# Kernel tuning notes

Measured on AMD Instinct MI355X. Metric: run time of the kernel, lower is better.

Reference implementation:

```python
import jax, jax.numpy as jnp
import numpy as np

B, N = 4096, 2048


def setup_inputs() -> dict:
    key = jax.random.key(0)
    k1, k2, k3 = jax.random.split(key, 3)
    target = jax.random.normal(k1, (B, N, 3), dtype=jnp.float32)
    source = jax.random.normal(k2, (B, N, 3), dtype=jnp.float32)
    weights = jax.random.uniform(k3, (B, N, 1), dtype=jnp.float32)
    return {"target": target, "source": source, "weights": weights}


def reference(target, source, weights):
    # Weighted means over the point axis (weights is not None branch of torch code;
    # the isnan mask is unused in that branch).
    wsum = jnp.sum(weights, axis=-2, keepdims=True) + 1e-8  # [B,1,1]
    mean_s = jnp.sum(source * weights, axis=-2, keepdims=True) / wsum  # [B,1,3]
    mean_t = jnp.sum(target * weights, axis=-2, keepdims=True) / wsum  # [B,1,3]
    xyz_tc = (target - mean_t) * weights  # weighted centered target [B,N,3]
    xyz_sc = source - mean_s              # centered source [B,N,3]
    # Cross-covariance: cov = xyz_tc^T @ xyz_sc -> [B,3,3]
    cov = jnp.einsum("bni,bnj->bij", xyz_tc, xyz_sc)
    u, s, vh = jnp.linalg.svd(cov, full_matrices=False)
    rot = u @ vh  # [B,3,3] (no reflection fix, matching original)
    t = jnp.swapaxes(mean_t, -1, -2) - rot @ jnp.swapaxes(mean_s, -1, -2)  # [B,3,1]
    T = jnp.zeros(target.shape[:-2] + (4, 4), dtype=target.dtype)
    T = T.at[..., :3, :3].set(rot)
    T = T.at[..., :3, 3:].set(t)
    T = T.at[..., 3, 3].set(jnp.asarray(1.0, target.dtype))
    return T
```

## Files before the change

### kernel.cpp

```cpp
#include <hip/hip_runtime.h>
#include <math.h>


constexpr int BN      = 2048;
constexpr int THREADS = 256;

__global__ __launch_bounds__(THREADS) void moments_kernel(
    const float* __restrict__ target,
    const float* __restrict__ source,
    const float* __restrict__ weights,
    float* __restrict__ ws)
{
    const int lane = threadIdx.x & 63;
    const int b    = (blockIdx.x * THREADS + threadIdx.x) >> 6;

    const float4* t4 = reinterpret_cast<const float4*>(target + (size_t)b * BN * 3);
    const float4* s4 = reinterpret_cast<const float4*>(source + (size_t)b * BN * 3);
    const float4* w4 = reinterpret_cast<const float4*>(weights + (size_t)b * BN);

    float acc[16];
#pragma unroll
    for (int i = 0; i < 16; ++i) acc[i] = 0.f;

#pragma unroll
    for (int it = 0; it < BN / (64 * 4); ++it) {
        const int g  = it * 64 + lane;
        float4 t0 = t4[g * 3 + 0], t1 = t4[g * 3 + 1], t2 = t4[g * 3 + 2];
        float4 s0 = s4[g * 3 + 0], s1 = s4[g * 3 + 1], s2 = s4[g * 3 + 2];
        float4 wv = w4[g];

        float tx[4] = {t0.x, t0.w, t1.z, t2.y};
        float ty[4] = {t0.y, t1.x, t1.w, t2.z};
        float tz[4] = {t0.z, t1.y, t2.x, t2.w};
        float sx[4] = {s0.x, s0.w, s1.z, s2.y};
        float sy[4] = {s0.y, s1.x, s1.w, s2.z};
        float sz[4] = {s0.z, s1.y, s2.x, s2.w};
        float ww[4] = {wv.x, wv.y, wv.z, wv.w};

#pragma unroll
        for (int j = 0; j < 4; ++j) {
            float w = ww[j];
            acc[0] += w;
            float wtx = w * tx[j], wty = w * ty[j], wtz = w * tz[j];
            acc[1] += wtx;  acc[2] += wty;  acc[3] += wtz;
            acc[4] += w * sx[j]; acc[5] += w * sy[j]; acc[6] += w * sz[j];
            acc[7]  += wtx * sx[j]; acc[8]  += wtx * sy[j]; acc[9]  += wtx * sz[j];
            acc[10] += wty * sx[j]; acc[11] += wty * sy[j]; acc[12] += wty * sz[j];
            acc[13] += wtz * sx[j]; acc[14] += wtz * sy[j]; acc[15] += wtz * sz[j];
        }
    }

#pragma unroll
    for (int i = 0; i < 16; ++i) {
#pragma unroll
        for (int off = 32; off > 0; off >>= 1)
            acc[i] += __shfl_xor(acc[i], off);
    }

    if (lane == 0) {
        float4* o = reinterpret_cast<float4*>(ws + (size_t)b * 16);
        o[0] = make_float4(acc[0],  acc[1],  acc[2],  acc[3]);
        o[1] = make_float4(acc[4],  acc[5],  acc[6],  acc[7]);
        o[2] = make_float4(acc[8],  acc[9],  acc[10], acc[11]);
        o[3] = make_float4(acc[12], acc[13], acc[14], acc[15]);
    }
}

__global__ __launch_bounds__(64) void polar_kernel(
    const float* __restrict__ ws,
    float* __restrict__ out,
    int B)
{
    const int b = blockIdx.x * 64 + threadIdx.x;
    if (b >= B) return;

    const float4* i4 = reinterpret_cast<const float4*>(ws + (size_t)b * 16);
    float4 p0 = i4[0], p1 = i4[1], p2 = i4[2], p3 = i4[3];
    double v[16] = {p0.x, p0.y, p0.z, p0.w,  p1.x, p1.y, p1.z, p1.w,
                    p2.x, p2.y, p2.z, p2.w,  p3.x, p3.y, p3.z, p3.w};

    const double W  = v[0];
    const double Wd = W + 1e-8;
    double St[3] = {v[1], v[2], v[3]};
    double Ss[3] = {v[4], v[5], v[6]};
    double mt[3], ms[3];
#pragma unroll
    for (int i = 0; i < 3; ++i) { mt[i] = St[i] / Wd; ms[i] = Ss[i] / Wd; }

    double A[3][3];
#pragma unroll
    for (int i = 0; i < 3; ++i)
#pragma unroll
        for (int j = 0; j < 3; ++j)
            A[i][j] = v[7 + i * 3 + j] - mt[i] * Ss[j] - ms[j] * St[i] + mt[i] * ms[j] * W;

    double X[3][3];
#pragma unroll
    for (int i = 0; i < 3; ++i)
#pragma unroll
        for (int j = 0; j < 3; ++j) X[i][j] = A[i][j];

#pragma unroll
    for (int iter = 0; iter < 12; ++iter) {
        double C[3][3];
        C[0][0] = X[1][1]*X[2][2] - X[1][2]*X[2][1];
        C[0][1] = X[1][2]*X[2][0] - X[1][0]*X[2][2];
        C[0][2] = X[1][0]*X[2][1] - X[1][1]*X[2][0];
        C[1][0] = X[0][2]*X[2][1] - X[0][1]*X[2][2];
        C[1][1] = X[0][0]*X[2][2] - X[0][2]*X[2][0];
        C[1][2] = X[0][1]*X[2][0] - X[0][0]*X[2][1];
        C[2][0] = X[0][1]*X[1][2] - X[0][2]*X[1][1];
        C[2][1] = X[0][2]*X[1][0] - X[0][0]*X[1][2];
        C[2][2] = X[0][0]*X[1][1] - X[0][1]*X[1][0];
        double det = X[0][0]*C[0][0] + X[0][1]*C[0][1] + X[0][2]*C[0][2];
        double ad  = fabs(det);
        if (!(ad > 1e-300)) { det = (det >= 0.0) ? 1e-300 : -1e-300; ad = 1e-300; }

        double mu = 1.0;
        if (iter < 9) {
            float adf = (float)ad;
            if (adf > 0.f && isfinite(adf))
                mu = (double)exp2f(-log2f(adf) * (1.0f / 3.0f));
        }
        double k1 = 0.5 * mu;
        double k2 = 0.5 / (mu * det);
#pragma unroll
        for (int i = 0; i < 3; ++i)
#pragma unroll
            for (int j = 0; j < 3; ++j)
                X[i][j] = k1 * X[i][j] + k2 * C[i][j];
    }

    double tvec[3];
#pragma unroll
    for (int i = 0; i < 3; ++i) {
        double s = mt[i];
#pragma unroll
        for (int k = 0; k < 3; ++k) s -= X[i][k] * ms[k];
        tvec[i] = s;
    }

    float4* o = reinterpret_cast<float4*>(out + (size_t)b * 16);
    o[0] = make_float4((float)X[0][0], (float)X[0][1], (float)X[0][2], (float)tvec[0]);
    o[1] = make_float4((float)X[1][0], (float)X[1][1], (float)X[1][2], (float)tvec[1]);
    o[2] = make_float4((float)X[2][0], (float)X[2][1], (float)X[2][2], (float)tvec[2]);
    o[3] = make_float4(0.f, 0.f, 0.f, 1.f);
}

extern "C" void kernel_launch(void* const* d_in, const int* in_sizes, int n_in,
                              void* d_out, int out_size, void* d_ws, size_t ws_size,
                              hipStream_t stream) {
    const float* target  = (const float*)d_in[0];
    const float* source  = (const float*)d_in[1];
    const float* weights = (const float*)d_in[2];
    float* out = (float*)d_out;
    float* ws  = (float*)d_ws;

    const int B = in_sizes[2] / BN;

    moments_kernel<<<B / (THREADS / 64), THREADS, 0, stream>>>(target, source, weights, ws);
    polar_kernel<<<(B + 63) / 64, 64, 0, stream>>>(ws, out, B);
}
```

Baseline: 43.57 us.

## Split each batch's point reduction across two wavefronts with a transpose-style shuffle reduce

```diff
diff --git a/kernel.cpp b/kernel.cpp
--- a/kernel.cpp
+++ b/kernel.cpp
@@ -2,29 +2,35 @@
 #include <math.h>
 
 
-constexpr int BN      = 2048;
-constexpr int THREADS = 256;
-
-__global__ __launch_bounds__(THREADS) void moments_kernel(
+constexpr int BN = 2048;
+
+template <int SPLIT>
+__global__ __launch_bounds__(256) void moments_kernel(
     const float* __restrict__ target,
     const float* __restrict__ source,
     const float* __restrict__ weights,
     float* __restrict__ ws)
 {
     const int lane = threadIdx.x & 63;
-    const int b    = (blockIdx.x * THREADS + threadIdx.x) >> 6;
+    const int wid  = blockIdx.x * 4 + (threadIdx.x >> 6);
+    const int b    = wid / SPLIT;
+    const int part = wid % SPLIT;
+
+    constexpr int GROUPS = BN / 4;
+    constexpr int ITERS  = GROUPS / (SPLIT * 64);
 
     const float4* t4 = reinterpret_cast<const float4*>(target + (size_t)b * BN * 3);
     const float4* s4 = reinterpret_cast<const float4*>(source + (size_t)b * BN * 3);
     const float4* w4 = reinterpret_cast<const float4*>(weights + (size_t)b * BN);
+    const int pg0 = part * (GROUPS / SPLIT);
 
     float acc[16];
 #pragma unroll
     for (int i = 0; i < 16; ++i) acc[i] = 0.f;
 
 #pragma unroll
-    for (int it = 0; it < BN / (64 * 4); ++it) {
-        const int g  = it * 64 + lane;
+    for (int it = 0; it < ITERS; ++it) {
+        const int g = pg0 + it * 64 + lane;
         float4 t0 = t4[g * 3 + 0], t1 = t4[g * 3 + 1], t2 = t4[g * 3 + 2];
         float4 s0 = s4[g * 3 + 0], s1 = s4[g * 3 + 1], s2 = s4[g * 3 + 2];
         float4 wv = w4[g];
@@ -50,34 +56,65 @@
         }
     }
 
-#pragma unroll
-    for (int i = 0; i < 16; ++i) {
-#pragma unroll
-        for (int off = 32; off > 0; off >>= 1)
-            acc[i] += __shfl_xor(acc[i], off);
-    }
-
-    if (lane == 0) {
-        float4* o = reinterpret_cast<float4*>(ws + (size_t)b * 16);
-        o[0] = make_float4(acc[0],  acc[1],  acc[2],  acc[3]);
-        o[1] = make_float4(acc[4],  acc[5],  acc[6],  acc[7]);
-        o[2] = make_float4(acc[8],  acc[9],  acc[10], acc[11]);
-        o[3] = make_float4(acc[12], acc[13], acc[14], acc[15]);
-    }
+    {
+        const bool u5 = (lane & 32) != 0;
+#pragma unroll
+        for (int v = 0; v < 8; ++v) {
+            float send = u5 ? acc[v] : acc[v + 8];
+            float r = __shfl_xor(send, 32);
+            acc[v] = (u5 ? acc[v + 8] : acc[v]) + r;
+        }
+        const bool u4 = (lane & 16) != 0;
+#pragma unroll
+        for (int v = 0; v < 4; ++v) {
+            float send = u4 ? acc[v] : acc[v + 4];
+            float r = __shfl_xor(send, 16);
+            acc[v] = (u4 ? acc[v + 4] : acc[v]) + r;
+        }
+        const bool u3 = (lane & 8) != 0;
+#pragma unroll
+        for (int v = 0; v < 2; ++v) {
+            float send = u3 ? acc[v] : acc[v + 2];
+            float r = __shfl_xor(send, 8);
+            acc[v] = (u3 ? acc[v + 2] : acc[v]) + r;
+        }
+        const bool u2 = (lane & 4) != 0;
+        {
+            float send = u2 ? acc[0] : acc[1];
+            float r = __shfl_xor(send, 4);
+            acc[0] = (u2 ? acc[1] : acc[0]) + r;
+        }
+        acc[0] += __shfl_xor(acc[0], 2);
+        acc[0] += __shfl_xor(acc[0], 1);
+    }
+
+    const int aidx = (((lane >> 5) & 1) << 3) | (((lane >> 4) & 1) << 2) |
+                     (((lane >> 3) & 1) << 1) | ((lane >> 2) & 1);
+    if ((lane & 3) == 0)
+        ws[((size_t)b * SPLIT + part) * 16 + aidx] = acc[0];
 }
 
-__global__ __launch_bounds__(64) void polar_kernel(
+template <int SPLIT>
+__global__ __launch_bounds__(256) void polar_kernel(
     const float* __restrict__ ws,
     float* __restrict__ out,
     int B)
 {
-    const int b = blockIdx.x * 64 + threadIdx.x;
+    const int b = blockIdx.x * 256 + threadIdx.x;
     if (b >= B) return;
 
-    const float4* i4 = reinterpret_cast<const float4*>(ws + (size_t)b * 16);
-    float4 p0 = i4[0], p1 = i4[1], p2 = i4[2], p3 = i4[3];
-    double v[16] = {p0.x, p0.y, p0.z, p0.w,  p1.x, p1.y, p1.z, p1.w,
-                    p2.x, p2.y, p2.z, p2.w,  p3.x, p3.y, p3.z, p3.w};
+    double v[16];
+#pragma unroll
+    for (int i = 0; i < 16; ++i) v[i] = 0.0;
+#pragma unroll
+    for (int p = 0; p < SPLIT; ++p) {
+        const float4* i4 = reinterpret_cast<const float4*>(ws + ((size_t)b * SPLIT + p) * 16);
+        float4 p0 = i4[0], p1 = i4[1], p2 = i4[2], p3 = i4[3];
+        float f[16] = {p0.x, p0.y, p0.z, p0.w,  p1.x, p1.y, p1.z, p1.w,
+                       p2.x, p2.y, p2.z, p2.w,  p3.x, p3.y, p3.z, p3.w};
+#pragma unroll
+        for (int i = 0; i < 16; ++i) v[i] += (double)f[i];
+    }
 
     const double W  = v[0];
     const double Wd = W + 1e-8;
@@ -158,6 +195,11 @@
 
     const int B = in_sizes[2] / BN;
 
-    moments_kernel<<<B / (THREADS / 64), THREADS, 0, stream>>>(target, source, weights, ws);
-    polar_kernel<<<(B + 63) / 64, 64, 0, stream>>>(ws, out, B);
+    if (ws_size >= (size_t)B * 2 * 16 * sizeof(float)) {
+        moments_kernel<2><<<B * 2 / 4, 256, 0, stream>>>(target, source, weights, ws);
+        polar_kernel<2><<<(B + 255) / 256, 256, 0, stream>>>(ws, out, B);
+    } else {
+        moments_kernel<1><<<B / 4, 256, 0, stream>>>(target, source, weights, ws);
+        polar_kernel<1><<<(B + 255) / 256, 256, 0, stream>>>(ws, out, B);
+    }
 }
```

New measurement: 43.62 us. Within noise of the previous version (+0.1%).
